# Kernel optimization log

Measured on AMD Instinct MI355X. Metric: run time of the kernel, lower is better.

The kernel has to match this reference:

```python
import jax, jax.numpy as jnp
import numpy as np

DIM = 8          # per-head dim
EPS = 1e-15
GROUPS_PW = 192  # 3 * heads = 3 * 64


def _conv(x, w, groups=1, pad=0):
    return jax.lax.conv_general_dilated(
        x, w, window_strides=(1, 1), padding=[(pad, pad), (pad, pad)],
        dimension_numbers=('NCHW', 'OIHW', 'NCHW'), feature_group_count=groups)


def setup_inputs() -> dict:
    key = jax.random.key(0)
    k0, k1, k2, k3, k4 = jax.random.split(key, 5)
    B, C, H, W = 4, 512, 64, 64
    td = 512  # heads * dim
    x = jax.random.normal(k0, (B, C, H, W), jnp.float32)
    w_qkv = jax.random.normal(k1, (3 * td, C, 1, 1), jnp.float32) * 0.05
    w_dw = jax.random.normal(k2, (3 * td, 1, 5, 5), jnp.float32) * 0.05
    w_pw = jax.random.normal(k3, (3 * td, (3 * td) // GROUPS_PW, 1, 1), jnp.float32) * 0.05
    w_proj = jax.random.normal(k4, (C, 2 * td, 1, 1), jnp.float32) * 0.05
    return {'x': x, 'w_qkv': w_qkv, 'w_dw': w_dw, 'w_pw': w_pw, 'w_proj': w_proj}


def reference(x, w_qkv, w_dw, w_pw, w_proj):
    # qkv projection (1x1 conv, no bias, no norm/act per config)
    qkv = _conv(x, w_qkv)  # [B, 3*td, H, W]
    # multi-scale aggregation: depthwise 5x5 then grouped 1x1 (groups = 3*heads)
    agg = _conv(_conv(qkv, w_dw, groups=w_dw.shape[0], pad=2), w_pw, groups=GROUPS_PW)
    qkv = jnp.concatenate([qkv, agg], axis=1)  # [B, 6*td, H, W]

    B, _, H, W = qkv.shape
    qkv = qkv.reshape(B, -1, 3 * DIM, H * W)  # [B, h_eff, 3*dim, HW]
    q = jax.nn.relu(qkv[:, :, :DIM])          # [B, h, dim, HW]
    k = jax.nn.relu(qkv[:, :, DIM:2 * DIM])   # [B, h, dim, HW]
    v = qkv[:, :, 2 * DIM:]                   # [B, h, dim, HW]
    # pad v with a row of ones -> normalization trick
    v = jnp.pad(v, ((0, 0), (0, 0), (0, 1), (0, 0)), constant_values=1.0)
    # linear attention via associativity: (v k^T) q
    vk = jnp.einsum('bhdn,bhen->bhde', v, k)   # [B, h, dim+1, dim]
    out = jnp.einsum('bhde,bhen->bhdn', vk, q) # [B, h, dim+1, HW]
    out = out[:, :, :-1] / (out[:, :, -1:] + EPS)
    out = out.reshape(B, -1, H, W)             # [B, 2*td, H, W]
    return x + _conv(out, w_proj)
```

## Files before the change

kernel.cpp:

```cpp
#include <hip/hip_runtime.h>
#include <hip/hip_bf16.h>
#include <cstdint>
#include <cstddef>


typedef __hip_bfloat16 bf16;
typedef __attribute__((ext_vector_type(8))) short short8;
typedef __attribute__((ext_vector_type(4))) float f32x4;

__device__ __forceinline__ float b2f(bf16 v) { return __bfloat162float(v); }
__device__ __forceinline__ bf16 f2b(float v) { return __float2bfloat16(v); }
__device__ __forceinline__ float us2f(unsigned short u) {
    return __uint_as_float(((unsigned)u) << 16);
}

__device__ __forceinline__ float dot2bf(unsigned p, unsigned wp, float acc) {
#if __has_builtin(__builtin_amdgcn_fdot2_f32_bf16)
    typedef __attribute__((ext_vector_type(2))) __bf16 bf16x2;
    return __builtin_amdgcn_fdot2_f32_bf16(
        __builtin_bit_cast(bf16x2, p), __builtin_bit_cast(bf16x2, wp),
        acc, false);
#else
    return acc
        + us2f((unsigned short)(p & 0xffffu))  * us2f((unsigned short)(wp & 0xffffu))
        + us2f((unsigned short)(p >> 16))      * us2f((unsigned short)(wp >> 16));
#endif
}

__device__ __forceinline__ void async16(void* lds_base, const void* gaddr) {
    __builtin_amdgcn_global_load_lds(
        (const __attribute__((address_space(1))) unsigned int*)gaddr,
        (__attribute__((address_space(3))) unsigned int*)lds_base,
        16, 0, 0);
}

__global__ __launch_bounds__(256) void convert_kernel(
    const float* __restrict__ src, bf16* __restrict__ dst, int n)
{
    int i = blockIdx.x * 256 + threadIdx.x;
    if (i < n) dst[i] = f2b(src[i]);
}

__global__ __launch_bounds__(256) void transpose_x_kernel(
    const float* __restrict__ x, bf16* __restrict__ x_t)
{
    __shared__ bf16 tile[32][33];
    const int b = blockIdx.z;
    const int c0 = blockIdx.y * 32;
    const int n0 = blockIdx.x * 32;
    const int tx = threadIdx.x & 31, ty = threadIdx.x >> 5;
    #pragma unroll
    for (int i = 0; i < 32; i += 8)
        tile[ty + i][tx] = f2b(x[((size_t)b * 512 + c0 + ty + i) * 4096 + n0 + tx]);
    __syncthreads();
    #pragma unroll
    for (int i = 0; i < 32; i += 8)
        x_t[((size_t)b * 4096 + n0 + ty + i) * 512 + c0 + tx] = tile[tx][ty + i];
}

template <bool PROJ>
__global__ __launch_bounds__(256) void mfma_gemm_kernel(
    const bf16* __restrict__ A, const bf16* __restrict__ xt_or_qkv,
    const bf16* __restrict__ agg, const float* __restrict__ X,
    void* __restrict__ Cout, int M, int K)
{
    constexpr int N = 4096;
    constexpr int NBUF = PROJ ? 4 : 2;
    constexpr int D    = PROJ ? 2 : 1;
    constexpr int ASZ = 128 * 32;
    const int b = blockIdx.z;
    const int m_blk = blockIdx.y * 128;
    const int n_blk = blockIdx.x * 128;

    __shared__ short smem[NBUF * 2 * ASZ];

    const int tid = threadIdx.x;
    const int lane = tid & 63, wave = tid >> 6;
    const int wm = (wave >> 1) * 64, wn = (wave & 1) * 64;
    const int fm = lane & 15, fq = lane >> 4;

    f32x4 acc[4][4] = {};

    const short* Ag = (const short*)A;
    const short* Btg = PROJ ? nullptr
        : (const short*)(xt_or_qkv + (size_t)b * N * 512);

    const int r_st = lane >> 2;
    const int cg_st = (lane & 3) ^ ((r_st >> 1) & 3);
    const int cx_rd = (fq ^ ((fm >> 1) & 3)) * 8;

    auto stage = [&](int buf, int k0) {
        short* Asb = &smem[buf * ASZ];
        short* Bsb = &smem[(NBUF + buf) * ASZ];
        #pragma unroll
        for (int t0 = 0; t0 < 2; ++t0) {
            int t = wave + t0 * 4;
            int row = m_blk + t * 16 + r_st;
            int col = k0 + cg_st * 8;
            async16(&Asb[t * 512], Ag + (size_t)row * K + col);
        }
        #pragma unroll
        for (int t0 = 0; t0 < 2; ++t0) {
            int t = wave + t0 * 4;
            int n = n_blk + t * 16 + r_st;
            if (!PROJ) {
                int col = k0 + cg_st * 8;
                async16(&Bsb[t * 512], Btg + (size_t)n * 512 + col);
            } else {
                int h = (k0 >> 3) + cg_st;
                const bf16* chunk = (h < 64 ? xt_or_qkv : agg) +
                    ((size_t)b * 1536 + (size_t)(h & 63) * 24 + 16) * 4096;
                async16(&Bsb[t * 512], chunk + (size_t)n * 8);
            }
        }
    };

    const int nt = K >> 5;
    stage(0, 0);
    if (D == 2 && nt > 1) stage(1, 32);

    for (int t = 0; t < nt; ++t) {
        if (D == 2 && t < nt - 1)
            asm volatile("s_waitcnt vmcnt(4)" ::: "memory");
        else
            asm volatile("s_waitcnt vmcnt(0)" ::: "memory");
        __builtin_amdgcn_s_barrier();
        if (t + D < nt) stage((t + D) & (NBUF - 1), (t + D) * 32);

        const int cb = t & (NBUF - 1);
        const short* Asb = &smem[cb * ASZ];
        const short* Bsb = &smem[(NBUF + cb) * ASZ];
        short8 af[4], bfv[4];
        #pragma unroll
        for (int i = 0; i < 4; ++i)
            af[i] = *(const short8*)&Asb[(wm + i * 16 + fm) * 32 + cx_rd];
        #pragma unroll
        for (int j = 0; j < 4; ++j)
            bfv[j] = *(const short8*)&Bsb[(wn + j * 16 + fm) * 32 + cx_rd];
        #pragma unroll
        for (int i = 0; i < 4; ++i)
            #pragma unroll
            for (int j = 0; j < 4; ++j)
                acc[i][j] = __builtin_amdgcn_mfma_f32_16x16x32_bf16(
                    af[i], bfv[j], acc[i][j], 0, 0, 0);
    }

    __syncthreads();
    float* zone = (float*)smem + wave * 1088;
    bf16* Cb  = PROJ ? nullptr : (bf16*)Cout + (size_t)b * M * N;
    float* Ob = PROJ ? (float*)Cout + (size_t)b * M * N : nullptr;
    const float* Xb = PROJ ? X + (size_t)b * M * N : nullptr;

    #pragma unroll
    for (int i = 0; i < 4; ++i) {
        #pragma unroll
        for (int j = 0; j < 4; ++j)
            #pragma unroll
            for (int r = 0; r < 4; ++r)
                zone[(fq * 4 + r) * 68 + j * 16 + fm] = acc[i][j][r];
        __syncthreads();

        #pragma unroll
        for (int p = 0; p < 2; ++p) {
            int idx = p * 64 + lane;
            int row = idx >> 3;
            int c0 = (idx & 7) * 8;
            f32x4 v0 = *(const f32x4*)&zone[row * 68 + c0];
            f32x4 v1 = *(const f32x4*)&zone[row * 68 + c0 + 4];
            int m = m_blk + wm + i * 16 + row;
            size_t off = (size_t)m * N + n_blk + wn + c0;
            if (!PROJ) {
                union { bf16 hv[8]; uint4 u; } pk;
                #pragma unroll
                for (int d = 0; d < 4; ++d) {
                    pk.hv[d] = f2b(v0[d]);
                    pk.hv[4 + d] = f2b(v1[d]);
                }
                *(uint4*)&Cb[off] = pk.u;
            } else {
                f32x4 x0 = *(const f32x4*)&Xb[off];
                f32x4 x1 = *(const f32x4*)&Xb[off + 4];
                *(f32x4*)&Ob[off]     = v0 + x0;
                *(f32x4*)&Ob[off + 4] = v1 + x1;
            }
        }
        __syncthreads();
    }
}

__global__ __launch_bounds__(256) void dwpw_kernel(
    const bf16* __restrict__ qkv, const float* __restrict__ w_dw,
    const float* __restrict__ w_pw, bf16* __restrict__ agg)
{
    const int bg = blockIdx.y;
    const int b = bg / 192;
    const int g = bg - b * 192;
    const int y0 = blockIdx.x * 32;

    __shared__ unsigned s_wdwp[8][16];
    __shared__ float s_wpw[8][8];

    const int tid = threadIdx.x;

    if (tid < 120) {
        int c = tid / 15, s = tid - c * 15;
        int i = s / 3, p = s - i * 3;
        int idx = i * 5 + p * 2;
        float w0 = w_dw[(size_t)(g * 8 + c) * 25 + idx];
        float w1 = (p < 2) ? w_dw[(size_t)(g * 8 + c) * 25 + idx + 1] : 0.f;
        unsigned u0 = __builtin_bit_cast(unsigned short, f2b(w0));
        unsigned u1 = __builtin_bit_cast(unsigned short, f2b(w1));
        s_wdwp[c][s] = u0 | (u1 << 16);
    }
    if (tid < 64)
        s_wpw[tid >> 3][tid & 7] = w_pw[(size_t)(g * 8 + (tid >> 3)) * 8 + (tid & 7)];
    __syncthreads();

    const int py = tid >> 3;
    const int sx = tid & 7;
    const int yq = y0 + py;
    const size_t chan_base = ((size_t)b * 1536 + g * 8) * 4096;

    const unsigned lo_keep = (sx > 0) ? 0xFFFFFFFFu : 0u;
    const unsigned hi_keep = (sx < 7) ? 0xFFFFFFFFu : 0u;

    float dwv[8][8];
    #pragma unroll
    for (int c = 0; c < 8; ++c) {
        unsigned wpq[16];
        #pragma unroll
        for (int q = 0; q < 4; ++q)
            *(uint4*)&wpq[q * 4] = *(const uint4*)&s_wdwp[c][q * 4];

        const char* cbase = (const char*)(qkv + chan_base + (size_t)c * 4096);
        float a[8] = {};
        #pragma unroll
        for (int i = 0; i < 5; ++i) {
            const int y = yq + i - 2;
            const bool row_ok = ((unsigned)y < 64u);
            const int yc = row_ok ? y : 0;
            const char* rowp = cbase + yc * 128;
            uint4 mid = *(const uint4*)(rowp + 16 * sx);
            const unsigned m = row_ok ? 0xFFFFFFFFu : 0u;

            unsigned lo = (unsigned)__shfl_up((int)mid.w, 1, 64);
            unsigned hi = (unsigned)__shfl_down((int)mid.x, 1, 64);

            unsigned W0 = lo & m & lo_keep;
            unsigned W1 = mid.x & m, W2 = mid.y & m;
            unsigned W3 = mid.z & m, W4 = mid.w & m;
            unsigned W5 = hi & m & hi_keep;
            unsigned S0 = __builtin_amdgcn_alignbit(W1, W0, 16);
            unsigned S1 = __builtin_amdgcn_alignbit(W2, W1, 16);
            unsigned S2 = __builtin_amdgcn_alignbit(W3, W2, 16);
            unsigned S3 = __builtin_amdgcn_alignbit(W4, W3, 16);
            unsigned S4 = __builtin_amdgcn_alignbit(W5, W4, 16);
            unsigned S5 = W5 >> 16;

            unsigned w01 = wpq[i * 3], w23 = wpq[i * 3 + 1], w4z = wpq[i * 3 + 2];
            a[0] = dot2bf(W0, w01, dot2bf(W1, w23, dot2bf(W2, w4z, a[0])));
            a[2] = dot2bf(W1, w01, dot2bf(W2, w23, dot2bf(W3, w4z, a[2])));
            a[4] = dot2bf(W2, w01, dot2bf(W3, w23, dot2bf(W4, w4z, a[4])));
            a[6] = dot2bf(W3, w01, dot2bf(W4, w23, dot2bf(W5, w4z, a[6])));
            a[1] = dot2bf(S0, w01, dot2bf(S1, w23, dot2bf(S2, w4z, a[1])));
            a[3] = dot2bf(S1, w01, dot2bf(S2, w23, dot2bf(S3, w4z, a[3])));
            a[5] = dot2bf(S2, w01, dot2bf(S3, w23, dot2bf(S4, w4z, a[5])));
            a[7] = dot2bf(S3, w01, dot2bf(S4, w23, dot2bf(S5, w4z, a[7])));
        }
        #pragma unroll
        for (int x = 0; x < 8; ++x) dwv[c][x] = a[x];
    }

    const size_t out_pix = (size_t)yq * 64 + 8 * sx;
    #pragma unroll
    for (int o = 0; o < 8; ++o) {
        float wv[8];
        *(float4*)&wv[0] = *(const float4*)&s_wpw[o][0];
        *(float4*)&wv[4] = *(const float4*)&s_wpw[o][4];
        float s[8] = {};
        #pragma unroll
        for (int i = 0; i < 8; ++i)
            #pragma unroll
            for (int x = 0; x < 8; ++x) s[x] += dwv[i][x] * wv[i];
        union { bf16 hv[8]; uint4 u; } pk;
        #pragma unroll
        for (int x = 0; x < 8; ++x) pk.hv[x] = f2b(s[x]);
        *(uint4*)(agg + chan_base + (size_t)o * 4096 + out_pix) = pk.u;
    }
}

__global__ __launch_bounds__(512) void vk_kernel(
    const bf16* __restrict__ qkv, const bf16* __restrict__ agg,
    float* __restrict__ vk)
{
    const int bh = blockIdx.x;
    const int b = bh >> 7;
    const int h = bh & 127;
    const bf16* base = (h < 64)
        ? (qkv + ((size_t)b * 1536 + h * 24) * 4096)
        : (agg + ((size_t)b * 1536 + (h - 64) * 24) * 4096);

    const int tid = threadIdx.x;
    const int n0 = tid * 8;

    short8 kr[8], vr[8];
    #pragma unroll
    for (int e = 0; e < 8; ++e)
        kr[e] = *(const short8*)&base[(size_t)(8 + e) * 4096 + n0];
    #pragma unroll
    for (int d = 0; d < 8; ++d)
        vr[d] = *(const short8*)&base[(size_t)(16 + d) * 4096 + n0];

    float acc[9][8] = {};
    #pragma unroll
    for (int t = 0; t < 8; ++t) {
        float kt[8], vt[8];
        #pragma unroll
        for (int e = 0; e < 8; ++e)
            kt[e] = fmaxf(us2f((unsigned short)kr[e][t]), 0.f);
        #pragma unroll
        for (int d = 0; d < 8; ++d)
            vt[d] = us2f((unsigned short)vr[d][t]);
        #pragma unroll
        for (int d = 0; d < 8; ++d)
            #pragma unroll
            for (int e = 0; e < 8; ++e)
                acc[d][e] += vt[d] * kt[e];
        #pragma unroll
        for (int e = 0; e < 8; ++e) acc[8][e] += kt[e];
    }

    __shared__ float red[8][72];
    const int lane = tid & 63, wave = tid >> 6;
    #pragma unroll
    for (int d = 0; d < 9; ++d) {
        #pragma unroll
        for (int e = 0; e < 8; ++e) {
            float v = acc[d][e];
            #pragma unroll
            for (int off = 32; off > 0; off >>= 1) v += __shfl_down(v, off, 64);
            if (lane == 0) red[wave][d * 8 + e] = v;
        }
    }
    __syncthreads();
    if (tid < 72) {
        float v = 0.f;
        #pragma unroll
        for (int w = 0; w < 8; ++w) v += red[w][tid];
        vk[(size_t)bh * 72 + tid] = v;
    }
}

__global__ __launch_bounds__(256) void attn_out_kernel(
    bf16* __restrict__ qkv, bf16* __restrict__ agg,
    const float* __restrict__ vk)
{
    const int b = blockIdx.z;
    const int h = blockIdx.y;
    const int n0 = (blockIdx.x * 256 + threadIdx.x) * 8;
    bf16* base = (h < 64)
        ? (qkv + ((size_t)b * 1536 + h * 24) * 4096)
        : (agg + ((size_t)b * 1536 + (h - 64) * 24) * 4096);

    __shared__ float s_vk[72];
    if (threadIdx.x < 72)
        s_vk[threadIdx.x] = vk[((size_t)b * 128 + h) * 72 + threadIdx.x];
    __syncthreads();

    short8 qr[8];
    #pragma unroll
    for (int e = 0; e < 8; ++e)
        qr[e] = *(const short8*)&base[(size_t)e * 4096 + n0];

    char* outp = (char*)(base + (size_t)16 * 4096) + (size_t)n0 * 16;
    #pragma unroll
    for (int t = 0; t < 8; ++t) {
        float q[8];
        #pragma unroll
        for (int e = 0; e < 8; ++e)
            q[e] = fmaxf(us2f((unsigned short)qr[e][t]), 0.f);

        float o[9];
        #pragma unroll
        for (int d = 0; d < 9; ++d) {
            float s = 0.f;
            #pragma unroll
            for (int e = 0; e < 8; ++e) s += s_vk[d * 8 + e] * q[e];
            o[d] = s;
        }
        const float denom = o[8] + 1e-15f;

        union { bf16 hv[8]; uint4 u; } pk;
        #pragma unroll
        for (int d = 0; d < 8; ++d) pk.hv[d] = f2b(o[d] / denom);
        *(uint4*)(outp + (size_t)t * 16) = pk.u;
    }
}

extern "C" void kernel_launch(void* const* d_in, const int* in_sizes, int n_in,
                              void* d_out, int out_size, void* d_ws, size_t ws_size,
                              hipStream_t stream) {
    const float* x      = (const float*)d_in[0];
    const float* w_qkv  = (const float*)d_in[1];
    const float* w_dw   = (const float*)d_in[2];
    const float* w_pw   = (const float*)d_in[3];
    const float* w_proj = (const float*)d_in[4];

    char* ws = (char*)d_ws;
    bf16* w_qkv_bf  = (bf16*)ws;
    bf16* w_proj_bf = (bf16*)(ws + 1572864);
    float* vkbf     = (float*)(ws + 1572864 + 1048576);
    bf16* x_t       = (bf16*)(ws + 1572864 + 1048576 + 147456);
    bf16* qkv       = x_t + (size_t)4 * 4096 * 512;
    bf16* agg       = qkv + (size_t)4 * 1536 * 4096;

    convert_kernel<<<3072, 256, 0, stream>>>(w_qkv, w_qkv_bf, 786432);
    convert_kernel<<<2048, 256, 0, stream>>>(w_proj, w_proj_bf, 524288);
    transpose_x_kernel<<<dim3(128, 16, 4), 256, 0, stream>>>(x, x_t);

    mfma_gemm_kernel<false><<<dim3(32, 12, 4), 256, 0, stream>>>(
        w_qkv_bf, x_t, nullptr, nullptr, qkv, 1536, 512);

    dwpw_kernel<<<dim3(2, 768), 256, 0, stream>>>(qkv, w_dw, w_pw, agg);

    vk_kernel<<<dim3(512), 512, 0, stream>>>(qkv, agg, vkbf);

    attn_out_kernel<<<dim3(2, 128, 4), 256, 0, stream>>>(qkv, agg, vkbf);

    mfma_gemm_kernel<true><<<dim3(32, 4, 4), 256, 0, stream>>>(
        w_proj_bf, qkv, agg, x, d_out, 512, 1024);
}
```

Baseline: 239.0 us.

## Fuse vk reduction with attention output and merge weight conversions

```diff
diff --git a/kernel.cpp b/kernel.cpp
--- a/kernel.cpp
+++ b/kernel.cpp
@@ -34,11 +34,13 @@
         16, 0, 0);
 }
 
-__global__ __launch_bounds__(256) void convert_kernel(
-    const float* __restrict__ src, bf16* __restrict__ dst, int n)
+__global__ __launch_bounds__(256) void convert2_kernel(
+    const float* __restrict__ a, bf16* __restrict__ da, int na,
+    const float* __restrict__ b2, bf16* __restrict__ db, int nb)
 {
     int i = blockIdx.x * 256 + threadIdx.x;
-    if (i < n) dst[i] = f2b(src[i]);
+    if (i < na)            da[i] = f2b(a[i]);
+    else if (i - na < nb)  db[i - na] = f2b(b2[i - na]);
 }
 
 __global__ __launch_bounds__(256) void transpose_x_kernel(
@@ -289,14 +291,13 @@
     }
 }
 
-__global__ __launch_bounds__(512) void vk_kernel(
-    const bf16* __restrict__ qkv, const bf16* __restrict__ agg,
-    float* __restrict__ vk)
+__global__ __launch_bounds__(512) void vk_attn_kernel(
+    bf16* __restrict__ qkv, bf16* __restrict__ agg)
 {
     const int bh = blockIdx.x;
     const int b = bh >> 7;
     const int h = bh & 127;
-    const bf16* base = (h < 64)
+    bf16* base = (h < 64)
         ? (qkv + ((size_t)b * 1536 + h * 24) * 4096)
         : (agg + ((size_t)b * 1536 + (h - 64) * 24) * 4096);
 
@@ -331,6 +332,7 @@
     }
 
     __shared__ float red[8][72];
+    __shared__ float s_vk[72];
     const int lane = tid & 63, wave = tid >> 6;
     #pragma unroll
     for (int d = 0; d < 9; ++d) {
@@ -347,24 +349,8 @@
         float v = 0.f;
         #pragma unroll
         for (int w = 0; w < 8; ++w) v += red[w][tid];
-        vk[(size_t)bh * 72 + tid] = v;
-    }
-}
-
-__global__ __launch_bounds__(256) void attn_out_kernel(
-    bf16* __restrict__ qkv, bf16* __restrict__ agg,
-    const float* __restrict__ vk)
-{
-    const int b = blockIdx.z;
-    const int h = blockIdx.y;
-    const int n0 = (blockIdx.x * 256 + threadIdx.x) * 8;
-    bf16* base = (h < 64)
-        ? (qkv + ((size_t)b * 1536 + h * 24) * 4096)
-        : (agg + ((size_t)b * 1536 + (h - 64) * 24) * 4096);
-
-    __shared__ float s_vk[72];
-    if (threadIdx.x < 72)
-        s_vk[threadIdx.x] = vk[((size_t)b * 128 + h) * 72 + threadIdx.x];
+        s_vk[tid] = v;
+    }
     __syncthreads();
 
     short8 qr[8];
@@ -409,13 +395,12 @@
     char* ws = (char*)d_ws;
     bf16* w_qkv_bf  = (bf16*)ws;
     bf16* w_proj_bf = (bf16*)(ws + 1572864);
-    float* vkbf     = (float*)(ws + 1572864 + 1048576);
     bf16* x_t       = (bf16*)(ws + 1572864 + 1048576 + 147456);
     bf16* qkv       = x_t + (size_t)4 * 4096 * 512;
     bf16* agg       = qkv + (size_t)4 * 1536 * 4096;
 
-    convert_kernel<<<3072, 256, 0, stream>>>(w_qkv, w_qkv_bf, 786432);
-    convert_kernel<<<2048, 256, 0, stream>>>(w_proj, w_proj_bf, 524288);
+    convert2_kernel<<<5120, 256, 0, stream>>>(
+        w_qkv, w_qkv_bf, 786432, w_proj, w_proj_bf, 524288);
     transpose_x_kernel<<<dim3(128, 16, 4), 256, 0, stream>>>(x, x_t);
 
     mfma_gemm_kernel<false><<<dim3(32, 12, 4), 256, 0, stream>>>(
@@ -423,9 +408,7 @@
 
     dwpw_kernel<<<dim3(2, 768), 256, 0, stream>>>(qkv, w_dw, w_pw, agg);
 
-    vk_kernel<<<dim3(512), 512, 0, stream>>>(qkv, agg, vkbf);
-
-    attn_out_kernel<<<dim3(2, 128, 4), 256, 0, stream>>>(qkv, agg, vkbf);
+    vk_attn_kernel<<<dim3(512), 512, 0, stream>>>(qkv, agg);
 
     mfma_gemm_kernel<true><<<dim3(32, 4, 4), 256, 0, stream>>>(
         w_proj_bf, qkv, agg, x, d_out, 512, 1024);
```

Result: slower. 247.1 us (+3.4%).
